# Kernel tuning notes

Hardware: AMD Instinct MI355X
Metric: run time of the kernel (lower is better)

Reference implementation:

```python
import jax, jax.numpy as jnp
import numpy as np

B, L = 2, 4096
EMBED_DIM, NUM_HEADS, WINDOW = 1024, 16, 256
NUM_EXPERTS, TOP_K, FF_HIDDEN = 8, 2, 4096
ENTROPY_W, MAX_USAGE = 0.1, 0.3


def setup_inputs() -> dict:
    key = jax.random.key(0)
    ks = jax.random.split(key, 10)
    s = 0.02
    C, F, E = EMBED_DIM, FF_HIDDEN, NUM_EXPERTS
    return {
        "x": jax.random.normal(ks[0], (B, L, C), jnp.float32),
        "g1": jnp.ones((C,), jnp.float32), "b1": jnp.zeros((C,), jnp.float32),
        "g2": jnp.ones((C,), jnp.float32), "b2": jnp.zeros((C,), jnp.float32),
        "g3": jnp.ones((C,), jnp.float32), "b3": jnp.zeros((C,), jnp.float32),
        "Wqkv": jax.random.normal(ks[1], (C, 3 * C), jnp.float32) * s, "bqkv": jnp.zeros((3 * C,), jnp.float32),
        "Wo": jax.random.normal(ks[2], (C, C), jnp.float32) * s, "bo": jnp.zeros((C,), jnp.float32),
        "conv_w": jax.random.normal(ks[3], (C, C, 3), jnp.float32) * s, "conv_b": jnp.zeros((C,), jnp.float32),
        "gate_W": jax.random.normal(ks[4], (C, E), jnp.float32) * s, "gate_b": jnp.zeros((E,), jnp.float32),
        "expert_W": jax.random.normal(ks[5], (E, C, C), jnp.float32) * s, "expert_b": jnp.zeros((E, C), jnp.float32),
        "ff_W1": jax.random.normal(ks[6], (C, F), jnp.float32) * s, "ff_b1": jnp.zeros((F,), jnp.float32),
        "ff_W2": jax.random.normal(ks[7], (F, C), jnp.float32) * s, "ff_b2": jnp.zeros((C,), jnp.float32),
    }


def _ln(x, g, b):
    mu = x.mean(-1, keepdims=True)
    var = ((x - mu) ** 2).mean(-1, keepdims=True)
    return (x - mu) * jax.lax.rsqrt(var + 1e-5) * g + b


def _local_attn(x, Wqkv, bqkv, Wo, bo):
    # Faithful port of the unfold-based overlapping-window attention
    Bsz, Ln, C = x.shape
    hd = C // NUM_HEADS
    pad = (-Ln) % WINDOW
    xp = jnp.pad(x, ((0, 0), (0, pad), (0, 0)))
    Lp = Ln + pad
    qkv = (xp @ Wqkv + bqkv).reshape(Bsz, Lp, 3, NUM_HEADS, hd).transpose(2, 0, 3, 1, 4)
    q, k, v = qkv[0], qkv[1], qkv[2]  # [B,H,Lp,hd]
    step = WINDOW // 2  # bidirectional=True -> overlapping windows
    nw = (Lp - WINDOW) // step + 1
    idx = (jnp.arange(nw) * step)[:, None] + jnp.arange(WINDOW)[None, :]  # [nw,w]

    def win(t):
        # torch unfold(dim=2,size=w,step) puts window on LAST axis -> [B,H,nw,hd,w]
        return jnp.swapaxes(t[:, :, idx, :], -1, -2)

    qw, kw, vw = win(q), win(k), win(v)
    # q @ k^T over the window axis (exactly what the torch code computes)
    attn = jax.nn.softmax(jnp.einsum('bhnds,bhnes->bhnde', qw, kw) * hd ** -0.5, axis=-1)
    o = jnp.einsum('bhnde,bhnes->bhnds', attn, vw)  # [B,H,nw,hd,w]
    o = o.reshape(Bsz, NUM_HEADS, nw * WINDOW, hd).transpose(0, 2, 1, 3).reshape(Bsz, nw * WINDOW, C)
    return (o @ Wo + bo)[:, :Ln]


def _dconv(x, w, b):
    # Conv1d(C,C,k=3,dilation=2,padding='same'); w is [O,I,K]
    y = jax.lax.conv_general_dilated(jnp.swapaxes(x, 1, 2), w, (1,), 'SAME',
                                     rhs_dilation=(2,), dimension_numbers=('NCH', 'OIH', 'NCH'))
    return jnp.swapaxes(y + b[None, :, None], 1, 2)


def _moe(x, gW, gb, eW, eb):
    Bsz, S, C = x.shape
    N = Bsz * S
    xf = x.reshape(N, C)
    probs = jax.nn.softmax(xf @ gW + gb, axis=-1)
    entropy = -jnp.sum(probs * jnp.log(probs + 1e-10), axis=-1).mean()
    topk_p, topk_i = jax.lax.top_k(probs, TOP_K)  # [N,K]
    # dense-equivalent top-k dispatch: out[n] = sum_k p_k * expert_{i_k}(x_n)
    eo = jnp.einsum('nc,ech->neh', xf, eW) + eb  # [N,E,C]
    combine = jnp.zeros((N, NUM_EXPERTS), xf.dtype).at[jnp.arange(N)[:, None], topk_i].add(topk_p)
    out = jnp.einsum('neh,ne->nh', eo, combine)
    counts = jnp.zeros((NUM_EXPERTS,), jnp.float32).at[topk_i.reshape(-1)].add(1.0)
    penalty = jnp.sum(jax.nn.relu(counts / N - MAX_USAGE))
    return out.reshape(Bsz, S, C), ENTROPY_W * entropy + penalty


def reference(x, g1, b1, g2, b2, g3, b3, Wqkv, bqkv, Wo, bo, conv_w, conv_b,
              gate_W, gate_b, expert_W, expert_b, ff_W1, ff_b1, ff_W2, ff_b2):
    x = x + _local_attn(_ln(x, g1, b1), Wqkv, bqkv, Wo, bo)
    x = x + _dconv(_ln(x, g2, b2), conv_w, conv_b)
    moe_out, aux = _moe(_ln(x, g3, b3), gate_W, gate_b, expert_W, expert_b)
    x = x + moe_out
    x = x + (jax.nn.gelu(x @ ff_W1 + ff_b1, approximate=False) @ ff_W2 + ff_b2)
    return x, aux
```

## Files before the change

kernel.cpp:

```cpp
#include <hip/hip_runtime.h>
#include <cmath>

typedef _Float16 f16;
typedef __attribute__((ext_vector_type(8))) _Float16 f16x8;
typedef __attribute__((ext_vector_type(4))) _Float16 f16x4;
typedef __attribute__((ext_vector_type(4))) float f32x4;

struct TileInfo { int m0, mcnt, e, pad; };

__device__ __forceinline__ void gload16(const void* g, void* l) {
  __builtin_amdgcn_global_load_lds((const __attribute__((address_space(1))) void*)g,
                                   (__attribute__((address_space(3))) void*)l, 16, 0, 0);
}

__device__ __forceinline__ float fast_gelu(float u) {
  const float c = u * (0.7978845608028654f + 0.0356774081f * u * u);
  const float t = fminf(2.0f * c, 80.0f);
  const float e = __expf(t);
  return u * (e * __builtin_amdgcn_rcpf(e + 1.0f));
}

template<int NPASS, int MODE, int EPI>
__global__ __launch_bounds__(256)
void gemm_kernel(const f16* __restrict__ Ah, const f16* __restrict__ Al, int lda,
                 const f16* __restrict__ Bh, const f16* __restrict__ Bl, int ldb,
                 const float* __restrict__ bias, const float* __restrict__ res,
                 float* __restrict__ outf, f16* __restrict__ outh, int ldo, int K,
                 const int* __restrict__ rowmap, const TileInfo* __restrict__ table,
                 const char* __restrict__ zbuf) {
  constexpr int BK = 64;
  constexpr int RB = 128;
  constexpr int TB = 16384;
  constexpr int ROUNDS = 4;
  constexpr int TPR = 8;
  constexpr int RPR = 32;
  constexpr int SWM = 7;
  constexpr int LA  = 0;
  constexpr int LAL = (NPASS == 3) ? TB : 0;
  constexpr int LB  = (NPASS == 3) ? 2 * TB : TB;
  constexpr int LBL = (NPASS == 3) ? 3 * TB : 0;

  __shared__ __align__(16) char lds[65536];

  const int tid  = threadIdx.x;
  const int wave = tid >> 6;
  const int lane = tid & 63;

  int m0, mcnt, eidx = 0;
  if (MODE == 2) {
    TileInfo ti = table[blockIdx.x];
    if (ti.mcnt <= 0) return;
    m0 = ti.m0; mcnt = ti.mcnt; eidx = ti.e;
  } else { m0 = blockIdx.x * 128; mcnt = 128; }
  const int n0 = blockIdx.y * 128;

  const f16* Bh_ = Bh;
  const float* bias_ = bias;
  size_t adelta = 0, bdelta = 0;
  if (NPASS == 3) {
    adelta = (size_t)((const char*)Al - (const char*)Ah);
    bdelta = (size_t)((const char*)Bl - (const char*)Bh);
  }
  if (MODE == 2) { Bh_ += ((size_t)eidx << 20); bias_ += eidx * 1024; }

  const int sr    = tid / TPR;
  const int cbyte = (tid % TPR) * 16;

  const char* aSrc[ROUNDS];
  const char* bSrc[ROUNDS];
  int aRowC[ROUNDS]; int aCbs[ROUNDS];
  #pragma unroll
  for (int r = 0; r < ROUNDS; ++r) {
    const int mr  = sr + r * RPR;
    const int cbs = cbyte ^ ((mr & SWM) << 4);
    int gi = m0 + ((mr < mcnt) ? mr : (mcnt - 1));
    if (MODE == 1 || MODE == 2) gi = rowmap[gi];
    if (MODE == 3) { aRowC[r] = gi; aCbs[r] = cbs; aSrc[r] = nullptr; }
    else           { aSrc[r] = (const char*)Ah + (size_t)gi * lda * 2 + cbs; aRowC[r] = 0; aCbs[r] = 0; }
    const int nr   = sr + r * RPR;
    const int ncbs = cbyte ^ ((nr & SWM) << 4);
    bSrc[r] = (const char*)Bh_ + (size_t)(n0 + nr) * ldb * 2 + ncbs;
  }

  f32x4 acc[4][4] = {};
  const int wm  = (wave >> 1) * 64;
  const int wn  = (wave & 1) * 64;
  const int fr  = lane & 15;
  const int kgb = (lane >> 4) * 16;

  if constexpr (NPASS == 1) {
    const int NT = K / BK;
    #pragma unroll
    for (int r = 0; r < ROUNDS; ++r) {
      gload16(aSrc[r], lds + r * 4096 + wave * 1024);
      gload16(bSrc[r], lds + 16384 + r * 4096 + wave * 1024);
    }
    #pragma unroll
    for (int r = 0; r < ROUNDS; ++r) {
      gload16(aSrc[r] + (size_t)BK * 2, lds + 32768 + r * 4096 + wave * 1024);
      gload16(bSrc[r] + (size_t)BK * 2, lds + 32768 + 16384 + r * 4096 + wave * 1024);
    }
    asm volatile("s_waitcnt vmcnt(8)" ::: "memory");
    __builtin_amdgcn_s_barrier();

    for (int kt = 0; kt < NT; ++kt) {
      const int c = kt & 1;
      const char* LAp = lds + c * 32768;
      const char* LBp = LAp + 16384;
      f16x8 ah[2][4], bh[2][4];
      #pragma unroll
      for (int kk = 0; kk < 2; ++kk) {
        #pragma unroll
        for (int i = 0; i < 4; ++i) {
          const int ar = wm + i * 16 + fr;
          ah[kk][i] = *(const f16x8*)(LAp + ar * RB + ((kk * 64 + kgb) ^ ((ar & SWM) << 4)));
          const int br = wn + i * 16 + fr;
          bh[kk][i] = *(const f16x8*)(LBp + br * RB + ((kk * 64 + kgb) ^ ((br & SWM) << 4)));
        }
      }
      asm volatile("s_waitcnt lgkmcnt(0)" ::: "memory");
      __builtin_amdgcn_s_barrier();
      if (kt + 2 < NT) {
        const size_t ko = (size_t)(kt + 2) * BK * 2;
        #pragma unroll
        for (int r = 0; r < ROUNDS; ++r) {
          gload16(aSrc[r] + ko, lds + c * 32768 + r * 4096 + wave * 1024);
          gload16(bSrc[r] + ko, lds + c * 32768 + 16384 + r * 4096 + wave * 1024);
        }
      }
      #pragma unroll
      for (int kk = 0; kk < 2; ++kk)
        #pragma unroll
        for (int i = 0; i < 4; ++i)
          #pragma unroll
          for (int j = 0; j < 4; ++j)
            acc[i][j] = __builtin_amdgcn_mfma_f32_16x16x32_f16(ah[kk][i], bh[kk][j], acc[i][j], 0, 0, 0);
      if (kt + 2 < NT) asm volatile("s_waitcnt vmcnt(8)" ::: "memory");
      else             asm volatile("s_waitcnt vmcnt(0)" ::: "memory");
      __builtin_amdgcn_s_barrier();
    }
  } else {
    for (int k0 = 0; k0 < K; k0 += BK) {
      #pragma unroll
      for (int r = 0; r < ROUNDS; ++r) {
        const char* as;
        const char* asl = nullptr;
        if (MODE == 3) {
          const int tap = k0 >> 10;
          const int kc  = k0 & 1023;
          const int tok = aRowC[r] & 4095;
          const int st  = tok + (tap - 1) * 2;
          if (st >= 0 && st < 4096) {
            as  = (const char*)Ah + (size_t)(aRowC[r] + (tap - 1) * 2) * 2048 + kc * 2 + aCbs[r];
            asl = as + adelta;
          } else {
            as  = zbuf;
            asl = zbuf;
          }
        } else {
          as  = aSrc[r] + (size_t)k0 * 2;
          asl = as + adelta;
        }
        gload16(as, lds + LA + r * 4096 + wave * 1024);
        gload16(asl, lds + LAL + r * 4096 + wave * 1024);
        const char* bs = bSrc[r] + (size_t)k0 * 2;
        gload16(bs, lds + LB + r * 4096 + wave * 1024);
        gload16(bs + bdelta, lds + LBL + r * 4096 + wave * 1024);
      }
      __syncthreads();
      #pragma unroll
      for (int kk = 0; kk < 2; ++kk) {
        f16x8 ah[4], bh[4], al[4], bl[4];
        #pragma unroll
        for (int i = 0; i < 4; ++i) {
          const int ar = wm + i * 16 + fr;
          const int ao = ar * RB + ((kk * 64 + kgb) ^ ((ar & SWM) << 4));
          ah[i] = *(const f16x8*)(lds + LA + ao);
          al[i] = *(const f16x8*)(lds + LAL + ao);
          const int br = wn + i * 16 + fr;
          const int bo = br * RB + ((kk * 64 + kgb) ^ ((br & SWM) << 4));
          bh[i] = *(const f16x8*)(lds + LB + bo);
          bl[i] = *(const f16x8*)(lds + LBL + bo);
        }
        #pragma unroll
        for (int i = 0; i < 4; ++i) {
          #pragma unroll
          for (int j = 0; j < 4; ++j) {
            acc[i][j] = __builtin_amdgcn_mfma_f32_16x16x32_f16(ah[i], bh[j], acc[i][j], 0, 0, 0);
            acc[i][j] = __builtin_amdgcn_mfma_f32_16x16x32_f16(ah[i], bl[j], acc[i][j], 0, 0, 0);
            acc[i][j] = __builtin_amdgcn_mfma_f32_16x16x32_f16(al[i], bh[j], acc[i][j], 0, 0, 0);
          }
        }
      }
      __syncthreads();
    }
  }

  #pragma unroll
  for (int i = 0; i < 4; ++i) {
    const int mb = wm + i * 16 + (lane >> 4) * 4;
    #pragma unroll
    for (int j = 0; j < 4; ++j) {
      const int nc = n0 + wn + j * 16 + fr;
      const float bv = bias_[nc];
      #pragma unroll
      for (int q = 0; q < 4; ++q) {
        const int ml = mb + q;
        if (MODE == 2 && ml >= mcnt) continue;
        const size_t orow = (size_t)(m0 + ml);
        float v = acc[i][j][q] + bv;
        if (EPI == 1) v += res[orow * ldo + nc];
        if (EPI == 3) v = fast_gelu(v);
        if (EPI <= 1) outf[orow * ldo + nc] = v;
        else          outh[orow * ldo + nc] = (f16)v;
      }
    }
  }
}

template<int WLO, int WGATE>
__global__ __launch_bounds__(256)
void ln_kernel(const float* __restrict__ x, const float* __restrict__ g, const float* __restrict__ b,
               f16* __restrict__ oh, f16* __restrict__ ol,
               const float* __restrict__ gW, const float* __restrict__ gb,
               float* __restrict__ logits) {
  const int row = blockIdx.x;
  const int t = threadIdx.x;
  const float4 v = ((const float4*)(x + (size_t)row * 1024))[t];
  float s  = v.x + v.y + v.z + v.w;
  float ss = v.x * v.x + v.y * v.y + v.z * v.z + v.w * v.w;
  #pragma unroll
  for (int off = 32; off; off >>= 1) { s += __shfl_down(s, off, 64); ss += __shfl_down(ss, off, 64); }
  __shared__ float red[8];
  if ((t & 63) == 0) { red[t >> 6] = s; red[(t >> 6) + 4] = ss; }
  __syncthreads();
  s  = red[0] + red[1] + red[2] + red[3];
  ss = red[4] + red[5] + red[6] + red[7];
  const float mu  = s * (1.0f / 1024.0f);
  const float var = ss * (1.0f / 1024.0f) - mu * mu;
  const float inv = 1.0f / sqrtf(var + 1e-5f);
  const float4 gv = ((const float4*)g)[t];
  const float4 bv = ((const float4*)b)[t];
  float y[4];
  y[0] = (v.x - mu) * inv * gv.x + bv.x;
  y[1] = (v.y - mu) * inv * gv.y + bv.y;
  y[2] = (v.z - mu) * inv * gv.z + bv.z;
  y[3] = (v.w - mu) * inv * gv.w + bv.w;
  f16x4 hv;
  #pragma unroll
  for (int u = 0; u < 4; ++u) hv[u] = (f16)y[u];
  *(f16x4*)(oh + (size_t)row * 1024 + t * 4) = hv;
  if (WLO) {
    f16x4 lv;
    #pragma unroll
    for (int u = 0; u < 4; ++u) lv[u] = (f16)(y[u] - (float)hv[u]);
    *(f16x4*)(ol + (size_t)row * 1024 + t * 4) = lv;
  }
  if (WGATE) {
    const float* gr = gW + (size_t)(t * 4) * 8;
    float lg[8];
    #pragma unroll
    for (int e = 0; e < 8; ++e)
      lg[e] = y[0] * gr[e] + y[1] * gr[8 + e] + y[2] * gr[16 + e] + y[3] * gr[24 + e];
    #pragma unroll
    for (int m = 1; m < 64; m <<= 1)
      #pragma unroll
      for (int e = 0; e < 8; ++e) lg[e] += __shfl_xor(lg[e], m, 64);
    __shared__ float gred[4][8];
    if ((t & 63) == 0) {
      #pragma unroll
      for (int e = 0; e < 8; ++e) gred[t >> 6][e] = lg[e];
    }
    __syncthreads();
    if (t < 8)
      logits[(size_t)row * 8 + t] = gred[0][t] + gred[1][t] + gred[2][t] + gred[3][t] + gb[t];
  }
}

__global__ __launch_bounds__(512, 4)
void attn_kernel(const float* __restrict__ qkv, f16* __restrict__ oh, f16* __restrict__ ol) {
  __shared__ __align__(16) char sm[81920];
  const int bid = blockIdx.x;
  const int b = bid >> 8, h = (bid >> 4) & 15, n = bid & 15;
  const int t = threadIdx.x;
  const size_t rowbase = (size_t)(b * 2176 + n * 128);
  const char* qg = (const char*)(qkv + rowbase * 3072 + h * 64);
  const char* kg = qg + 4096;
  const char* vg = qg + 8192;

  const int srow = t >> 4;
  const int scol = (t & 15) * 16;
  const int wuni = (t >> 6) * 1024;

  const int dt = t >> 4;
  const int et = t & 15;
  float pacc[2][4] = {};

  for (int r = 0; r < 2; ++r) {
    #pragma unroll
    for (int p = 0; p < 4; ++p) {
      const size_t off = (size_t)(r * 128 + p * 32 + srow) * 12288 + scol;
      gload16(qg + off, sm + p * 8192 + wuni);
      gload16(kg + off, sm + 32768 + p * 8192 + wuni);
    }
    __syncthreads();
    #pragma unroll 4
    for (int s = 0; s < 128; ++s) {
      const float2 q2 = *(const float2*)(sm + s * 256 + dt * 8);
      const f32x4 k4 = *(const f32x4*)(sm + 32768 + s * 256 + et * 16);
      #pragma unroll
      for (int z = 0; z < 4; ++z) {
        pacc[0][z] += q2.x * k4[z];
        pacc[1][z] += q2.y * k4[z];
      }
    }
    __syncthreads();
  }

  #pragma unroll
  for (int i = 0; i < 2; ++i) {
    #pragma unroll
    for (int z = 0; z < 4; ++z) pacc[i][z] *= 0.125f;
    float m = fmaxf(fmaxf(pacc[i][0], pacc[i][1]), fmaxf(pacc[i][2], pacc[i][3]));
    m = fmaxf(m, __shfl_xor(m, 1, 16));
    m = fmaxf(m, __shfl_xor(m, 2, 16));
    m = fmaxf(m, __shfl_xor(m, 4, 16));
    m = fmaxf(m, __shfl_xor(m, 8, 16));
    float den = 0.0f;
    #pragma unroll
    for (int z = 0; z < 4; ++z) { pacc[i][z] = __expf(pacc[i][z] - m); den += pacc[i][z]; }
    den += __shfl_xor(den, 1, 16);
    den += __shfl_xor(den, 2, 16);
    den += __shfl_xor(den, 4, 16);
    den += __shfl_xor(den, 8, 16);
    const float dinv = 1.0f / den;
    f32x4 pv;
    #pragma unroll
    for (int z = 0; z < 4; ++z) pv[z] = pacc[i][z] * dinv;
    *(f32x4*)(sm + 65536 + (dt * 2 + i) * 256 + et * 16) = pv;
  }

  const int dt2 = t & 15;
  const int st  = t >> 4;
  const int ch  = h * 64 + (st & 15) * 4;
  const size_t rb2 = (size_t)(b * 4096 + n * 256);

  for (int c = 0; c < 2; ++c) {
    __syncthreads();
    #pragma unroll
    for (int p = 0; p < 4; ++p) {
      const size_t off = (size_t)(c * 128 + p * 32 + srow) * 12288 + scol;
      gload16(vg + off, sm + p * 8192 + wuni);
    }
    __syncthreads();
    float o[16];
    #pragma unroll
    for (int u = 0; u < 16; ++u) o[u] = 0.0f;
    #pragma unroll 2
    for (int e4 = 0; e4 < 16; ++e4) {
      f32x4 p4[4], v4[4];
      #pragma unroll
      for (int i = 0; i < 4; ++i)
        p4[i] = *(const f32x4*)(sm + 65536 + (dt2 * 4 + i) * 256 + e4 * 16);
      #pragma unroll
      for (int j = 0; j < 4; ++j)
        v4[j] = *(const f32x4*)(sm + (st * 4 + j) * 256 + e4 * 16);
      #pragma unroll
      for (int j = 0; j < 4; ++j)
        #pragma unroll
        for (int i = 0; i < 4; ++i) {
          o[j * 4 + i] += v4[j][0] * p4[i][0] + v4[j][1] * p4[i][1]
                        + v4[j][2] * p4[i][2] + v4[j][3] * p4[i][3];
        }
    }
    const int rq = c * 2 + (st >> 4);
    #pragma unroll
    for (int i = 0; i < 4; ++i) {
      const size_t row = rb2 + (size_t)(dt2 * 4 + i) * 4 + rq;
      f16x4 hv, lv;
      #pragma unroll
      for (int j = 0; j < 4; ++j) {
        const float val = o[j * 4 + i];
        hv[j] = (f16)val;
        lv[j] = (f16)(val - (float)hv[j]);
      }
      *(f16x4*)(oh + row * 1024 + ch) = hv;
      *(f16x4*)(ol + row * 1024 + ch) = lv;
    }
  }
}

template<int SPLIT>
__global__ __launch_bounds__(256)
void transpose_kernel(const float* __restrict__ in, int R, int Cc,
                      f16* __restrict__ oh, f16* __restrict__ ol) {
  __shared__ float tile[32][33];
  const size_t mat = (size_t)blockIdx.z * R * Cc;
  in += mat; oh += mat; if (SPLIT) ol += mat;
  const int tx = threadIdx.x & 31, ty = threadIdx.x >> 5;
  const int c = blockIdx.x * 32 + tx;
  #pragma unroll
  for (int j = 0; j < 32; j += 8) {
    const int r = blockIdx.y * 32 + ty + j;
    tile[ty + j][tx] = in[(size_t)r * Cc + c];
  }
  __syncthreads();
  const int rT = blockIdx.y * 32 + tx;
  #pragma unroll
  for (int j = 0; j < 32; j += 8) {
    const int cT = blockIdx.x * 32 + ty + j;
    const float v = tile[tx][ty + j];
    const f16 hv = (f16)v;
    oh[(size_t)cT * R + rT] = hv;
    if (SPLIT) ol[(size_t)cT * R + rT] = (f16)(v - (float)hv);
  }
}

__global__ __launch_bounds__(256)
void convw_kernel(const float* __restrict__ w, f16* __restrict__ oh, f16* __restrict__ ol) {
  const int id = blockIdx.x * 256 + threadIdx.x;
  const int o = id >> 10, i = id & 1023;
  const float* ws = w + (size_t)o * 3072 + i * 3;
  #pragma unroll
  for (int tap = 0; tap < 3; ++tap) {
    const float v = ws[tap];
    const f16 hv = (f16)v;
    const size_t oi = (size_t)o * 3072 + tap * 1024 + i;
    oh[oi] = hv;
    ol[oi] = (f16)(v - (float)hv);
  }
}

__global__ void qkvrows_kernel(int* __restrict__ rows) {
  const int r = blockIdx.x * 256 + threadIdx.x;
  if (r < 4352) rows[r] = (r >= 2176) ? (4096 + r - 2176) : r;
}

__global__ __launch_bounds__(256)
void gatefin_kernel(const float* __restrict__ logits, float* __restrict__ top2p,
                    int* __restrict__ top2i, float* __restrict__ ent,
                    int* __restrict__ counts) {
  __shared__ int hist[8];
  const int t = threadIdx.x;
  if (t < 8) hist[t] = 0;
  __syncthreads();
  const int token = blockIdx.x * 256 + t;
  float lg[8];
  const float4 l0 = ((const float4*)(logits + (size_t)token * 8))[0];
  const float4 l1 = ((const float4*)(logits + (size_t)token * 8))[1];
  lg[0] = l0.x; lg[1] = l0.y; lg[2] = l0.z; lg[3] = l0.w;
  lg[4] = l1.x; lg[5] = l1.y; lg[6] = l1.z; lg[7] = l1.w;
  int i0 = 0; float v0 = lg[0];
  #pragma unroll
  for (int e = 1; e < 8; ++e) if (lg[e] > v0) { v0 = lg[e]; i0 = e; }
  int i1 = 0; float v1 = -1e30f;
  #pragma unroll
  for (int e = 0; e < 8; ++e) if (e != i0 && lg[e] > v1) { v1 = lg[e]; i1 = e; }
  float den = 0.0f; float pr[8];
  #pragma unroll
  for (int e = 0; e < 8; ++e) { pr[e] = __expf(lg[e] - v0); den += pr[e]; }
  const float dinv = 1.0f / den;
  float H = 0.0f, p0 = 0.0f, p1 = 0.0f;
  #pragma unroll
  for (int e = 0; e < 8; ++e) {
    const float p = pr[e] * dinv;
    H -= p * __logf(p + 1e-10f);
    if (e == i0) p0 = p;
    if (e == i1) p1 = p;
  }
  ent[token] = H;
  top2p[token * 2] = p0; top2p[token * 2 + 1] = p1;
  top2i[token * 2] = i0; top2i[token * 2 + 1] = i1;
  atomicAdd(&hist[i0], 1);
  atomicAdd(&hist[i1], 1);
  __syncthreads();
  if (t < 8) atomicAdd(&counts[t], hist[t]);
}

__global__ __launch_bounds__(256)
void scan_kernel(const float* __restrict__ ent, const int* __restrict__ counts,
                 int* __restrict__ offs, TileInfo* __restrict__ table, float* __restrict__ auxout) {
  __shared__ float red[256];
  const int t = threadIdx.x;
  float s = 0.0f;
  for (int k = 0; k < 32; ++k) s += ent[t + (k << 8)];
  red[t] = s; __syncthreads();
  for (int hh = 128; hh > 0; hh >>= 1) { if (t < hh) red[t] += red[t + hh]; __syncthreads(); }
  if (t == 0) {
    const float entmean = red[0] * (1.0f / 8192.0f);
    float pen = 0.0f; int off = 0; int nt = 0;
    for (int e = 0; e < 8; ++e) {
      const int c = counts[e];
      offs[e] = off;
      for (int m = 0; m < c; m += 128) {
        table[nt].m0 = off + m;
        table[nt].mcnt = (c - m < 128) ? (c - m) : 128;
        table[nt].e = e; table[nt].pad = 0;
        ++nt;
      }
      off += c;
      const float fr = (float)c * (1.0f / 8192.0f) - 0.3f;
      pen += (fr > 0.0f) ? fr : 0.0f;
    }
    for (; nt < 160; ++nt) { table[nt].m0 = 0; table[nt].mcnt = 0; table[nt].e = 0; table[nt].pad = 0; }
    auxout[0] = 0.1f * entmean + pen;
  }
}

__global__ __launch_bounds__(256)
void scatter_kernel(const int* __restrict__ top2i, const int* __restrict__ offs,
                    int* __restrict__ fill, int* __restrict__ moe_rows,
                    int* __restrict__ row2slot) {
  __shared__ int hist[8];
  __shared__ int base[8];
  const int t = threadIdx.x;
  if (t < 8) hist[t] = 0;
  __syncthreads();
  const int id = blockIdx.x * 256 + t;
  const int e = top2i[id];
  const int myrank = atomicAdd(&hist[e], 1);
  __syncthreads();
  if (t < 8) base[t] = atomicAdd(&fill[t], hist[t]);
  __syncthreads();
  const int row = offs[e] + base[e] + myrank;
  moe_rows[row] = id >> 1;
  row2slot[id] = row;
}

__global__ __launch_bounds__(256)
void combine_kernel(const float* __restrict__ x2, const f16* __restrict__ eo,
                    const float* __restrict__ top2p, const int* __restrict__ row2slot,
                    float* __restrict__ x3, f16* __restrict__ x3h) {
  const int n = blockIdx.x;
  const int t = threadIdx.x;
  const int r0 = row2slot[n * 2], r1 = row2slot[n * 2 + 1];
  const float p0 = top2p[n * 2], p1 = top2p[n * 2 + 1];
  const float4 xv = ((const float4*)(x2 + (size_t)n * 1024))[t];
  const f16x4 e0 = ((const f16x4*)(eo + (size_t)r0 * 1024))[t];
  const f16x4 e1 = ((const f16x4*)(eo + (size_t)r1 * 1024))[t];
  float4 o;
  o.x = xv.x + p0 * (float)e0[0] + p1 * (float)e1[0];
  o.y = xv.y + p0 * (float)e0[1] + p1 * (float)e1[1];
  o.z = xv.z + p0 * (float)e0[2] + p1 * (float)e1[2];
  o.w = xv.w + p0 * (float)e0[3] + p1 * (float)e1[3];
  ((float4*)(x3 + (size_t)n * 1024))[t] = o;
  f16x4 hv; hv[0] = (f16)o.x; hv[1] = (f16)o.y; hv[2] = (f16)o.z; hv[3] = (f16)o.w;
  ((f16x4*)(x3h + (size_t)n * 1024))[t] = hv;
}

extern "C" void kernel_launch(void* const* d_in, const int* in_sizes, int n_in,
                              void* d_out, int out_size, void* d_ws, size_t ws_size,
                              hipStream_t stream) {
  (void)in_sizes; (void)n_in; (void)out_size; (void)ws_size;
  const float* x     = (const float*)d_in[0];
  const float* g1    = (const float*)d_in[1];
  const float* b1    = (const float*)d_in[2];
  const float* g2    = (const float*)d_in[3];
  const float* b2    = (const float*)d_in[4];
  const float* g3    = (const float*)d_in[5];
  const float* b3    = (const float*)d_in[6];
  const float* Wqkv  = (const float*)d_in[7];
  const float* bqkv  = (const float*)d_in[8];
  const float* Wo    = (const float*)d_in[9];
  const float* bo    = (const float*)d_in[10];
  const float* convw = (const float*)d_in[11];
  const float* convb = (const float*)d_in[12];
  const float* gateW = (const float*)d_in[13];
  const float* gateb = (const float*)d_in[14];
  const float* expW  = (const float*)d_in[15];
  const float* expb  = (const float*)d_in[16];
  const float* ffW1  = (const float*)d_in[17];
  const float* ffb1  = (const float*)d_in[18];
  const float* ffW2  = (const float*)d_in[19];
  const float* ffb2  = (const float*)d_in[20];
  float* out = (float*)d_out;

  char* W = (char*)d_ws;
  f16* wqkvT_h = (f16*)(W + 0);
  f16* wqkvT_l = (f16*)(W + 6291456);
  f16* woT_h   = (f16*)(W + 12582912);
  f16* woT_l   = (f16*)(W + 14680064);
  f16* wcvT_h  = (f16*)(W + 16777216);
  f16* wcvT_l  = (f16*)(W + 23068672);
  f16* wexpT   = (f16*)(W + 29360128);
  f16* wff1T   = (f16*)(W + 46137344);
  f16* wff2T   = (f16*)(W + 54525952);
  char* META   = W + 62914560;
  int* counts    = (int*)(META);
  int* fill      = (int*)(META + 32);
  int* offs      = (int*)(META + 64);
  TileInfo* table = (TileInfo*)(META + 128);
  char* zbuf     = META + 3072;
  int* qkv_rows  = (int*)(META + 4096);
  float* ent     = (float*)(META + 24576);
  float* top2p   = (float*)(META + 57344);
  int* top2i     = (int*)(META + 122880);
  int* moe_rows  = (int*)(META + 188416);
  int* row2slot  = (int*)(META + 253952);
  float* logits  = (float*)(META + 327680);
  char* SA = W + 63963136;
  char* SB = W + 97517568;
  char* SC = W + 164626432;
  char* SD = W + 198180864;
  char* SE = W + 231735296;

  f16* ln1h = (f16*)SA;            f16* ln1l = (f16*)(SA + 16777216);
  f16* ln2h = ln1h;                f16* ln2l = ln1l;
  f16* ln3h = ln1h;                f16* x3h  = (f16*)(SA + 16777216);
  float* qkvbuf = (float*)SB;
  float* x2buf  = (float*)SB;
  f16*   hbuf   = (f16*)SB;
  f16* attnh = (f16*)SC;           f16* attnl = (f16*)(SC + 16777216);
  float* x1 = (float*)SD;
  f16* eobuf = (f16*)SD;
  float* x3 = (float*)SE;

  hipMemsetAsync((void*)META, 0, 4096, stream);

  dim3 blk(256);
  transpose_kernel<1><<<dim3(96, 32, 1), blk, 0, stream>>>(Wqkv, 1024, 3072, wqkvT_h, wqkvT_l);
  transpose_kernel<1><<<dim3(32, 32, 1), blk, 0, stream>>>(Wo, 1024, 1024, woT_h, woT_l);
  convw_kernel<<<4096, blk, 0, stream>>>(convw, wcvT_h, wcvT_l);
  transpose_kernel<0><<<dim3(32, 32, 8), blk, 0, stream>>>(expW, 1024, 1024, wexpT, nullptr);
  transpose_kernel<0><<<dim3(128, 32, 1), blk, 0, stream>>>(ffW1, 1024, 4096, wff1T, nullptr);
  transpose_kernel<0><<<dim3(32, 128, 1), blk, 0, stream>>>(ffW2, 4096, 1024, wff2T, nullptr);
  qkvrows_kernel<<<17, blk, 0, stream>>>(qkv_rows);

  ln_kernel<1, 0><<<8192, blk, 0, stream>>>(x, g1, b1, ln1h, ln1l, nullptr, nullptr, nullptr);
  gemm_kernel<3, 1, 0><<<dim3(34, 24), blk, 0, stream>>>(ln1h, ln1l, 1024, wqkvT_h, wqkvT_l, 1024,
      bqkv, nullptr, qkvbuf, nullptr, 3072, 1024, qkv_rows, nullptr, nullptr);
  attn_kernel<<<512, dim3(512), 0, stream>>>(qkvbuf, attnh, attnl);
  gemm_kernel<3, 0, 1><<<dim3(64, 8), blk, 0, stream>>>(attnh, attnl, 1024, woT_h, woT_l, 1024,
      bo, x, x1, nullptr, 1024, 1024, nullptr, nullptr, nullptr);
  ln_kernel<1, 0><<<8192, blk, 0, stream>>>(x1, g2, b2, ln2h, ln2l, nullptr, nullptr, nullptr);
  gemm_kernel<3, 3, 1><<<dim3(64, 8), blk, 0, stream>>>(ln2h, ln2l, 1024, wcvT_h, wcvT_l, 3072,
      convb, x1, x2buf, nullptr, 1024, 3072, nullptr, nullptr, zbuf);
  ln_kernel<0, 1><<<8192, blk, 0, stream>>>(x2buf, g3, b3, ln3h, nullptr, gateW, gateb, logits);
  gatefin_kernel<<<32, blk, 0, stream>>>(logits, top2p, top2i, ent, counts);
  scan_kernel<<<1, blk, 0, stream>>>(ent, counts, offs, table, out + 8388608);
  scatter_kernel<<<64, blk, 0, stream>>>(top2i, offs, fill, moe_rows, row2slot);
  gemm_kernel<1, 2, 2><<<dim3(136, 8), blk, 0, stream>>>(ln3h, nullptr, 1024, wexpT, nullptr, 1024,
      expb, nullptr, nullptr, eobuf, 1024, 1024, moe_rows, table, nullptr);
  combine_kernel<<<8192, blk, 0, stream>>>(x2buf, eobuf, top2p, row2slot, x3, x3h);
  gemm_kernel<1, 0, 3><<<dim3(64, 32), blk, 0, stream>>>(x3h, nullptr, 1024, wff1T, nullptr, 1024,
      ffb1, nullptr, nullptr, hbuf, 4096, 1024, nullptr, nullptr, nullptr);
  gemm_kernel<1, 0, 1><<<dim3(64, 8), blk, 0, stream>>>(hbuf, nullptr, 4096, wff2T, nullptr, 4096,
      ffb2, x3, out, nullptr, 1024, 4096, nullptr, nullptr, nullptr);
}
```

Baseline: 741.1 us.

## Double-buffer the 3-pass split-f16 GEMM path with BK=32 async prefetch

The 3-pass (hi/lo split) GEMM path used to load a full BK=64 tile of A, Alo, B and Blo into LDS and then synchronise before computing, so nothing overlapped. It now uses BK=32 tiles split into two 32 KB LDS buffers, with a new XOR swizzle for 64-byte rows. The tile two steps ahead is prefetched with global_load_lds while the current tile is computed, mirroring the 1-pass pipeline. The trade-off is twice as many k-iterations and barriers, plus a different bank-conflict pattern from the new swizzle.

Result: slower. 770.0 us (+3.9%).

```diff
diff --git a/kernel.cpp b/kernel.cpp
--- a/kernel.cpp
+++ b/kernel.cpp
@@ -28,18 +28,6 @@
                  float* __restrict__ outf, f16* __restrict__ outh, int ldo, int K,
                  const int* __restrict__ rowmap, const TileInfo* __restrict__ table,
                  const char* __restrict__ zbuf) {
-  constexpr int BK = 64;
-  constexpr int RB = 128;
-  constexpr int TB = 16384;
-  constexpr int ROUNDS = 4;
-  constexpr int TPR = 8;
-  constexpr int RPR = 32;
-  constexpr int SWM = 7;
-  constexpr int LA  = 0;
-  constexpr int LAL = (NPASS == 3) ? TB : 0;
-  constexpr int LB  = (NPASS == 3) ? 2 * TB : TB;
-  constexpr int LBL = (NPASS == 3) ? 3 * TB : 0;
-
   __shared__ __align__(16) char lds[65536];
 
   const int tid  = threadIdx.x;
@@ -63,42 +51,39 @@
   }
   if (MODE == 2) { Bh_ += ((size_t)eidx << 20); bias_ += eidx * 1024; }
 
-  const int sr    = tid / TPR;
-  const int cbyte = (tid % TPR) * 16;
-
-  const char* aSrc[ROUNDS];
-  const char* bSrc[ROUNDS];
-  int aRowC[ROUNDS]; int aCbs[ROUNDS];
-  #pragma unroll
-  for (int r = 0; r < ROUNDS; ++r) {
-    const int mr  = sr + r * RPR;
-    const int cbs = cbyte ^ ((mr & SWM) << 4);
-    int gi = m0 + ((mr < mcnt) ? mr : (mcnt - 1));
-    if (MODE == 1 || MODE == 2) gi = rowmap[gi];
-    if (MODE == 3) { aRowC[r] = gi; aCbs[r] = cbs; aSrc[r] = nullptr; }
-    else           { aSrc[r] = (const char*)Ah + (size_t)gi * lda * 2 + cbs; aRowC[r] = 0; aCbs[r] = 0; }
-    const int nr   = sr + r * RPR;
-    const int ncbs = cbyte ^ ((nr & SWM) << 4);
-    bSrc[r] = (const char*)Bh_ + (size_t)(n0 + nr) * ldb * 2 + ncbs;
-  }
-
   f32x4 acc[4][4] = {};
   const int wm  = (wave >> 1) * 64;
   const int wn  = (wave & 1) * 64;
   const int fr  = lane & 15;
   const int kgb = (lane >> 4) * 16;
+  const int wuni = wave * 1024;
 
   if constexpr (NPASS == 1) {
-    const int NT = K / BK;
-    #pragma unroll
-    for (int r = 0; r < ROUNDS; ++r) {
-      gload16(aSrc[r], lds + r * 4096 + wave * 1024);
-      gload16(bSrc[r], lds + 16384 + r * 4096 + wave * 1024);
-    }
-    #pragma unroll
-    for (int r = 0; r < ROUNDS; ++r) {
-      gload16(aSrc[r] + (size_t)BK * 2, lds + 32768 + r * 4096 + wave * 1024);
-      gload16(bSrc[r] + (size_t)BK * 2, lds + 32768 + 16384 + r * 4096 + wave * 1024);
+    const int sr    = tid / 8;
+    const int cbyte = (tid % 8) * 16;
+    const char* aSrc[4];
+    const char* bSrc[4];
+    #pragma unroll
+    for (int r = 0; r < 4; ++r) {
+      const int mr  = sr + r * 32;
+      const int cbs = cbyte ^ ((mr & 7) << 4);
+      int gi = m0 + ((mr < mcnt) ? mr : (mcnt - 1));
+      if (MODE == 1 || MODE == 2) gi = rowmap[gi];
+      aSrc[r] = (const char*)Ah + (size_t)gi * lda * 2 + cbs;
+      const int nr   = sr + r * 32;
+      const int ncbs = cbyte ^ ((nr & 7) << 4);
+      bSrc[r] = (const char*)Bh_ + (size_t)(n0 + nr) * ldb * 2 + ncbs;
+    }
+    const int NT = K / 64;
+    #pragma unroll
+    for (int r = 0; r < 4; ++r) {
+      gload16(aSrc[r], lds + r * 4096 + wuni);
+      gload16(bSrc[r], lds + 16384 + r * 4096 + wuni);
+    }
+    #pragma unroll
+    for (int r = 0; r < 4; ++r) {
+      gload16(aSrc[r] + 128, lds + 32768 + r * 4096 + wuni);
+      gload16(bSrc[r] + 128, lds + 32768 + 16384 + r * 4096 + wuni);
     }
     asm volatile("s_waitcnt vmcnt(8)" ::: "memory");
     __builtin_amdgcn_s_barrier();
@@ -113,19 +98,19 @@
         #pragma unroll
         for (int i = 0; i < 4; ++i) {
           const int ar = wm + i * 16 + fr;
-          ah[kk][i] = *(const f16x8*)(LAp + ar * RB + ((kk * 64 + kgb) ^ ((ar & SWM) << 4)));
+          ah[kk][i] = *(const f16x8*)(LAp + ar * 128 + ((kk * 64 + kgb) ^ ((ar & 7) << 4)));
           const int br = wn + i * 16 + fr;
-          bh[kk][i] = *(const f16x8*)(LBp + br * RB + ((kk * 64 + kgb) ^ ((br & SWM) << 4)));
+          bh[kk][i] = *(const f16x8*)(LBp + br * 128 + ((kk * 64 + kgb) ^ ((br & 7) << 4)));
         }
       }
       asm volatile("s_waitcnt lgkmcnt(0)" ::: "memory");
       __builtin_amdgcn_s_barrier();
       if (kt + 2 < NT) {
-        const size_t ko = (size_t)(kt + 2) * BK * 2;
+        const size_t ko = (size_t)(kt + 2) * 128;
         #pragma unroll
-        for (int r = 0; r < ROUNDS; ++r) {
-          gload16(aSrc[r] + ko, lds + c * 32768 + r * 4096 + wave * 1024);
-          gload16(bSrc[r] + ko, lds + c * 32768 + 16384 + r * 4096 + wave * 1024);
+        for (int r = 0; r < 4; ++r) {
+          gload16(aSrc[r] + ko, lds + c * 32768 + r * 4096 + wuni);
+          gload16(bSrc[r] + ko, lds + c * 32768 + 16384 + r * 4096 + wuni);
         }
       }
       #pragma unroll
@@ -140,59 +125,80 @@
       __builtin_amdgcn_s_barrier();
     }
   } else {
-    for (int k0 = 0; k0 < K; k0 += BK) {
-      #pragma unroll
-      for (int r = 0; r < ROUNDS; ++r) {
-        const char* as;
-        const char* asl = nullptr;
+    const int sr3 = tid >> 2;
+    const int cb3 = (tid & 3) * 16;
+    int aRow3[2], aCbs3[2], aOff3[2], bOff3[2];
+    #pragma unroll
+    for (int q = 0; q < 2; ++q) {
+      const int row = q * 64 + sr3;
+      const int cbs = cb3 ^ (((row >> 1) & 3) << 4);
+      int gi = m0 + row;
+      if (MODE == 1) gi = rowmap[m0 + row];
+      aRow3[q] = gi; aCbs3[q] = cbs;
+      aOff3[q] = gi * lda * 2 + cbs;
+      bOff3[q] = (n0 + row) * ldb * 2 + cbs;
+    }
+    const int NT = K / 32;
+
+    auto STAGE3 = [&](int kt2, char* bb) {
+      const int k0 = kt2 * 32;
+      #pragma unroll
+      for (int q = 0; q < 2; ++q) {
+        const char* as; const char* asl;
         if (MODE == 3) {
           const int tap = k0 >> 10;
           const int kc  = k0 & 1023;
-          const int tok = aRowC[r] & 4095;
+          const int tok = aRow3[q] & 4095;
           const int st  = tok + (tap - 1) * 2;
           if (st >= 0 && st < 4096) {
-            as  = (const char*)Ah + (size_t)(aRowC[r] + (tap - 1) * 2) * 2048 + kc * 2 + aCbs[r];
+            as  = (const char*)Ah + (size_t)(aRow3[q] + (tap - 1) * 2) * 2048 + kc * 2 + aCbs3[q];
             asl = as + adelta;
-          } else {
-            as  = zbuf;
-            asl = zbuf;
-          }
+          } else { as = zbuf; asl = zbuf; }
         } else {
-          as  = aSrc[r] + (size_t)k0 * 2;
+          as  = (const char*)Ah + (size_t)aOff3[q] + (size_t)k0 * 2;
           asl = as + adelta;
         }
-        gload16(as, lds + LA + r * 4096 + wave * 1024);
-        gload16(asl, lds + LAL + r * 4096 + wave * 1024);
-        const char* bs = bSrc[r] + (size_t)k0 * 2;
-        gload16(bs, lds + LB + r * 4096 + wave * 1024);
-        gload16(bs + bdelta, lds + LBL + r * 4096 + wave * 1024);
-      }
-      __syncthreads();
-      #pragma unroll
-      for (int kk = 0; kk < 2; ++kk) {
-        f16x8 ah[4], bh[4], al[4], bl[4];
+        gload16(as,  bb + q * 4096 + wuni);
+        gload16(asl, bb + 8192 + q * 4096 + wuni);
+        const char* bs = (const char*)Bh_ + (size_t)bOff3[q] + (size_t)k0 * 2;
+        gload16(bs,          bb + 16384 + q * 4096 + wuni);
+        gload16(bs + bdelta, bb + 24576 + q * 4096 + wuni);
+      }
+    };
+
+    STAGE3(0, lds);
+    STAGE3(1, lds + 32768);
+    asm volatile("s_waitcnt vmcnt(8)" ::: "memory");
+    __builtin_amdgcn_s_barrier();
+
+    for (int kt = 0; kt < NT; ++kt) {
+      char* bb = lds + (kt & 1) * 32768;
+      f16x8 ah[4], al[4], bh[4], bl[4];
+      #pragma unroll
+      for (int i = 0; i < 4; ++i) {
+        const int ar = wm + i * 16 + fr;
+        const int ao = ar * 64 + (kgb ^ (((ar >> 1) & 3) << 4));
+        ah[i] = *(const f16x8*)(bb + ao);
+        al[i] = *(const f16x8*)(bb + 8192 + ao);
+        const int br = wn + i * 16 + fr;
+        const int bo = br * 64 + (kgb ^ (((br >> 1) & 3) << 4));
+        bh[i] = *(const f16x8*)(bb + 16384 + bo);
+        bl[i] = *(const f16x8*)(bb + 24576 + bo);
+      }
+      asm volatile("s_waitcnt lgkmcnt(0)" ::: "memory");
+      __builtin_amdgcn_s_barrier();
+      if (kt + 2 < NT) STAGE3(kt + 2, bb);
+      #pragma unroll
+      for (int i = 0; i < 4; ++i)
         #pragma unroll
-        for (int i = 0; i < 4; ++i) {
-          const int ar = wm + i * 16 + fr;
-          const int ao = ar * RB + ((kk * 64 + kgb) ^ ((ar & SWM) << 4));
-          ah[i] = *(const f16x8*)(lds + LA + ao);
-          al[i] = *(const f16x8*)(lds + LAL + ao);
-          const int br = wn + i * 16 + fr;
-          const int bo = br * RB + ((kk * 64 + kgb) ^ ((br & SWM) << 4));
-          bh[i] = *(const f16x8*)(lds + LB + bo);
-          bl[i] = *(const f16x8*)(lds + LBL + bo);
+        for (int j = 0; j < 4; ++j) {
+          acc[i][j] = __builtin_amdgcn_mfma_f32_16x16x32_f16(ah[i], bh[j], acc[i][j], 0, 0, 0);
+          acc[i][j] = __builtin_amdgcn_mfma_f32_16x16x32_f16(ah[i], bl[j], acc[i][j], 0, 0, 0);
+          acc[i][j] = __builtin_amdgcn_mfma_f32_16x16x32_f16(al[i], bh[j], acc[i][j], 0, 0, 0);
         }
-        #pragma unroll
-        for (int i = 0; i < 4; ++i) {
-          #pragma unroll
-          for (int j = 0; j < 4; ++j) {
-            acc[i][j] = __builtin_amdgcn_mfma_f32_16x16x32_f16(ah[i], bh[j], acc[i][j], 0, 0, 0);
-            acc[i][j] = __builtin_amdgcn_mfma_f32_16x16x32_f16(ah[i], bl[j], acc[i][j], 0, 0, 0);
-            acc[i][j] = __builtin_amdgcn_mfma_f32_16x16x32_f16(al[i], bh[j], acc[i][j], 0, 0, 0);
-          }
-        }
-      }
-      __syncthreads();
+      if (kt + 2 < NT) asm volatile("s_waitcnt vmcnt(8)" ::: "memory");
+      else             asm volatile("s_waitcnt vmcnt(0)" ::: "memory");
+      __builtin_amdgcn_s_barrier();
     }
   }
 
```
